# Kernel optimization log

Hardware: AMD Instinct MI355X
Metric: run time of the kernel (lower is better)

## Reference

```python
import math
import jax, jax.numpy as jnp
import numpy as np

B, L, D, I, S, DTR, K, PH = 8, 2048, 512, 256, 8, 32, 3, 128


def setup_inputs() -> dict:
    key = jax.random.key(0)
    ks = jax.random.split(key, 12)
    def nrm(k, shape, s=0.02):
        return jax.random.normal(k, shape, jnp.float32) * s
    # dt_proj bias: inverse-softplus of exp(linspace(log 0.02, log 0.2))
    dt_init = np.exp(np.linspace(math.log(0.02), math.log(0.2), I))
    dt_b = np.log(np.expm1(dt_init)).astype(np.float32)
    A_log = np.log(np.tile(np.arange(1, S + 1, dtype=np.float32), (I, 1)))
    return dict(
        x=jax.random.normal(ks[0], (B, L, D), jnp.float32),
        position=jax.random.uniform(ks[1], (B, L, 6), jnp.float32),
        ln_in_w=jnp.ones(D, jnp.float32), ln_in_b=jnp.zeros(D, jnp.float32),
        pos_w1=nrm(ks[2], (PH, 6), 0.1), pos_b1=jnp.zeros(PH, jnp.float32),
        pos_w2=nrm(ks[3], (D, PH), 0.05), pos_b2=jnp.zeros(D, jnp.float32),
        scan_in_w=nrm(ks[4], (2, D, D)),
        scan_cx_w=nrm(ks[5], (2, I, 1, K), 0.2),
        scan_cz_w=nrm(ks[6], (2, I, 1, K), 0.2),
        scan_xp_w=nrm(ks[7], (2, DTR + 2 * S, I)),
        scan_dt_w=nrm(ks[8], (2, I, DTR)),
        scan_dt_b=jnp.tile(jnp.asarray(dt_b)[None], (2, 1)),
        scan_Alog=jnp.tile(jnp.asarray(A_log)[None], (2, 1, 1)),
        scan_Dp=jnp.ones((2, I), jnp.float32),
        scan_out_w=nrm(ks[9], (2, D, D)),  # zero-init in source; randomized for non-trivial testing
        mix_w=nrm(ks[10], (D, 3 * D)),
        ln_out_w=jnp.ones(D, jnp.float32), ln_out_b=jnp.zeros(D, jnp.float32),
    )


def _ln(x, w, b, eps=1e-6):
    m = x.mean(-1, keepdims=True)
    v = ((x - m) ** 2).mean(-1, keepdims=True)
    return (x - m) * jax.lax.rsqrt(v + eps) * w + b


def _dwconv_silu(x, w):
    # x: [B, L, C], w: [C, 1, K] depthwise conv1d, 'same' padding, then SiLU
    y = jax.lax.conv_general_dilated(
        jnp.swapaxes(x, 1, 2), w, (1,), ((K // 2, K // 2),),
        feature_group_count=w.shape[0], dimension_numbers=('NCH', 'OIH', 'NCH'))
    return jax.nn.silu(jnp.swapaxes(y, 1, 2))


def _selective_scan(x, in_w, cx_w, cz_w, xp_w, dt_w, dt_b, Alog, Dp, out_w):
    # ReferenceSelectiveScan1D.forward, x: [B, L, D]
    xb, zb = jnp.split(x @ in_w.T, 2, axis=-1)
    xb = _dwconv_silu(xb, cx_w)
    zb = _dwconv_silu(zb, cz_w)
    proj = xb @ xp_w.T  # [B, L, DTR + 2S]
    dt_raw, b_raw, c_raw = jnp.split(proj, [DTR, DTR + S], axis=-1)
    delta = jnp.clip(jax.nn.softplus(dt_raw @ dt_w.T + dt_b), 1e-4, 1.0)  # [B, L, I]
    bt = jnp.tanh(b_raw)  # [B, L, S]
    ct = jnp.tanh(c_raw)  # [B, L, S]
    a = jax.nn.softplus(Alog) + 1e-4  # [I, S]
    xs = (jnp.swapaxes(delta, 0, 1), jnp.swapaxes(bt, 0, 1),
          jnp.swapaxes(ct, 0, 1), jnp.swapaxes(xb, 0, 1))

    def step(state, inp):
        d_t, b_t, c_t, x_t = inp
        decay = jnp.clip(jnp.exp(-d_t[..., None] * a), 1e-4, 1.0)  # [B, I, S]
        state = decay * state + (1.0 - decay) * (b_t[:, None, :] * x_t[..., None])
        y = jnp.einsum('bis,bs->bi', state, c_t) + Dp * x_t
        return state, y

    state0 = jnp.zeros((x.shape[0], I, S), jnp.float32)
    _, ys = jax.lax.scan(step, state0, xs)  # ys: [L, B, I]
    y = jnp.swapaxes(ys, 0, 1)
    return jnp.concatenate([y, zb], -1) @ out_w.T


def reference(x, position, ln_in_w, ln_in_b, pos_w1, pos_b1, pos_w2, pos_b2,
              scan_in_w, scan_cx_w, scan_cz_w, scan_xp_w, scan_dt_w, scan_dt_b,
              scan_Alog, scan_Dp, scan_out_w, mix_w, ln_out_w, ln_out_b):
    pos = jax.nn.gelu(position @ pos_w1.T + pos_b1, approximate=False) @ pos_w2.T + pos_b2
    si = _ln(x, ln_in_w, ln_in_b) + pos
    params = lambda i: (scan_in_w[i], scan_cx_w[i], scan_cz_w[i], scan_xp_w[i],
                        scan_dt_w[i], scan_dt_b[i], scan_Alog[i], scan_Dp[i], scan_out_w[i])
    fwd = _selective_scan(si, *params(0))
    bwd = jnp.flip(_selective_scan(jnp.flip(si, 1), *params(1)), 1)
    mixed = jnp.concatenate([fwd, bwd, si], -1) @ mix_w.T
    return _ln(mixed, ln_out_w, ln_out_b)
```

## Files before the change

### kernel.cpp

```cpp
#include <hip/hip_runtime.h>
#include <hip/hip_bf16.h>

typedef __hip_bfloat16 bf16;
typedef __attribute__((ext_vector_type(8))) short short8;
typedef __attribute__((ext_vector_type(4))) float floatx4;

#define BBB 8
#define LL 2048
#define DDD 512
#define II 256
#define SS 8
#define MM (BBB*LL)
#define CHUNK 32
#define NCH (LL/CHUNK)

#define WS_SI    0l
#define WS_U0    16777216l
#define WS_U1    33554432l
#define WS_XZ    50331648l
#define WS_H     67108864l
#define WS_P     50331648l
#define WS_Q     58720256l
#define WS_SINB  67108864l
#define WS_XBC   83886080l
#define WS_MIXED 83886080l
#define WS_DELTA 100663296l
#define WS_BTCT  117440512l
#define WS_INWB  121634816l
#define WS_MIXWB 122683392l
#define WS_PW2B  124256256l
#define WS_OWT   124387328l
#define WS_WP    125435904l
#define WS_WD    126484480l
#define WS_XPWB  126746624l
#define WS_A2    126763008l
#define WS_WXT   126779392l
#define WS_WZT   126785536l
#define WS_MRS   126791680l
#define WS_LNBP  126922752l

__device__ __forceinline__ float b2f(unsigned short u) {
    return __uint_as_float(((unsigned)u) << 16);
}
__device__ __forceinline__ float bload(const bf16* p) {
    return b2f(*(const unsigned short*)p);
}
__device__ __forceinline__ void bstore(bf16* p, float v) {
    *p = __float2bfloat16(v);
}
__device__ __forceinline__ float softplus_f(float x) {
    return fmaxf(x, 0.f) + log1pf(expf(-fabsf(x)));
}
__device__ __forceinline__ float silu_f(float x) {
    return x / (1.f + expf(-x));
}
__device__ __forceinline__ void gl_lds16(const bf16* g, void* l) {
    __builtin_amdgcn_global_load_lds(
        (const __attribute__((address_space(1))) unsigned int*)g,
        (__attribute__((address_space(3))) unsigned int*)l, 16, 0, 0);
}
#define VMWAIT8() asm volatile("s_waitcnt vmcnt(8)" ::: "memory")
#define VMWAIT0() asm volatile("s_waitcnt vmcnt(0)" ::: "memory")
#define XBAR()    __builtin_amdgcn_s_barrier()

__device__ __forceinline__ void block_mean_rstd(float v0, float v1, float* red,
                                                float& mean, float& rstd) {
    float s = v0 + v1, q = v0*v0 + v1*v1;
    #pragma unroll
    for (int off = 32; off > 0; off >>= 1) {
        s += __shfl_down(s, off);
        q += __shfl_down(q, off);
    }
    int w = threadIdx.x >> 6, lane = threadIdx.x & 63;
    if (lane == 0) { red[w*2] = s; red[w*2+1] = q; }
    __syncthreads();
    if (threadIdx.x == 0) {
        float ts = 0.f, tq = 0.f;
        #pragma unroll
        for (int i = 0; i < 4; ++i) { ts += red[i*2]; tq += red[i*2+1]; }
        red[8] = ts; red[9] = tq;
    }
    __syncthreads();
    float ts = red[8], tq = red[9];
    mean = ts * (1.f/DDD);
    float var = tq * (1.f/DDD) - mean*mean;
    rstd = rsqrtf(var + 1e-6f);
}

__global__ __launch_bounds__(256)
void k_prep(const float* __restrict__ x, float* __restrict__ mrs,
            const float* __restrict__ lnb, const float* __restrict__ pb2,
            float* __restrict__ lnbp,
            const float* __restrict__ position, const float* __restrict__ pw1,
            const float* __restrict__ pb1, bf16* __restrict__ H,
            const float* __restrict__ ow, bf16* __restrict__ owT,
            const float* __restrict__ mixw, bf16* __restrict__ mixwb,
            const float* __restrict__ inw, bf16* __restrict__ inwb,
            const float* __restrict__ dtw, const float* __restrict__ xpw,
            bf16* __restrict__ Wd,
            const float* __restrict__ posw2, bf16* __restrict__ pw2b,
            bf16* __restrict__ xpwb,
            const float* __restrict__ Alog, float* __restrict__ a2,
            const float* __restrict__ cxw, const float* __restrict__ czw,
            float* __restrict__ wxT, float* __restrict__ wzT) {
    __shared__ float red[10];
    int bb = blockIdx.x;
    int tid = threadIdx.x;
    if (bb < 16384) {
        long row = bb;
        float v0 = x[row*DDD + tid], v1 = x[row*DDD + tid + 256];
        float mean, rstd;
        block_mean_rstd(v0, v1, red, mean, rstd);
        if (tid == 0) { mrs[row*2] = mean; mrs[row*2+1] = rstd; }
    } else if (bb < 24576) {
        long idx = (long)(bb - 16384)*256 + tid;
        long row = idx >> 7; int ph = idx & 127;
        const float* p = position + row*6;
        const float* w = pw1 + ph*6;
        float v = pb1[ph];
        #pragma unroll
        for (int j = 0; j < 6; ++j) v = fmaf(p[j], w[j], v);
        v = 0.5f * v * (1.f + erff(v * 0.70710678118654752440f));
        bstore(H + idx, v);
    } else if (bb < 26624) {
        long idx = (long)(bb - 24576)*256 + tid;
        long d = idx >> 18; long rem = idx & 262143;
        long k = rem >> 9, c = rem & 511;
        bstore(owT + idx, ow[d*262144 + c*512 + k]);
    } else if (bb < 27392) {
        int i = (bb - 26624)*256*4 + tid*4;
        float4 v = *(const float4*)(mixw + i);
        bf16 t[4] = {__float2bfloat16(v.x), __float2bfloat16(v.y),
                     __float2bfloat16(v.z), __float2bfloat16(v.w)};
        *(ushort4*)(mixwb + i) = *(ushort4*)t;
    } else if (bb < 27904) {
        int i = (bb - 27392)*256*4 + tid*4;
        float4 v = *(const float4*)(inw + i);
        bf16 t[4] = {__float2bfloat16(v.x), __float2bfloat16(v.y),
                     __float2bfloat16(v.z), __float2bfloat16(v.w)};
        *(ushort4*)(inwb + i) = *(ushort4*)t;
    } else if (bb < 28416) {
        int local = bb - 27904;
        int d = local >> 8, i = local & 255, j = tid;
        const float* wr = dtw + (long)d*II*32 + i*32;
        const float* xp = xpw + (long)d*48*II;
        float acc = 0.f;
        #pragma unroll
        for (int k = 0; k < 32; ++k) acc = fmaf(wr[k], xp[k*II + j], acc);
        bstore(Wd + ((long)d*II + i)*II + j, acc);
    } else if (bb < 28480) {
        int i = (bb - 28416)*256*4 + tid*4;
        float4 v = *(const float4*)(posw2 + i);
        bf16 t[4] = {__float2bfloat16(v.x), __float2bfloat16(v.y),
                     __float2bfloat16(v.z), __float2bfloat16(v.w)};
        *(ushort4*)(pw2b + i) = *(ushort4*)t;
    } else if (bb < 28512) {
        int idx = (bb - 28480)*256 + tid;
        int d = idx >> 12, rem = idx & 4095;
        bstore(xpwb + idx, xpw[(long)d*48*II + 32*II + rem]);
    } else if (bb < 28528) {
        int idx = (bb - 28512)*256 + tid;
        float a = softplus_f(Alog[idx]) + 1e-4f;
        a2[idx] = -1.4426950408889634f * a;
    } else if (bb < 28534) {
        int idx = (bb - 28528)*256 + tid;
        if (idx < 1536) {
            int d = idx / 768, rem = idx % 768;
            int k = rem >> 8, i = rem & 255;
            int kk = d ? (2 - k) : k;
            wxT[idx] = cxw[d*768 + i*3 + kk];
            wzT[idx] = czw[d*768 + i*3 + kk];
        }
    } else {
        int idx = (bb - 28534)*256 + tid;
        lnbp[idx] = lnb[idx] + pb2[idx];
    }
}

#define GEMM_COMPUTE(Sa, Sb)                                                      \
    do {                                                                          \
        _Pragma("unroll")                                                         \
        for (int kk = 0; kk < 2; ++kk) {                                          \
            const int sa_ = ((kk*4 + lq) ^ (lr & 7)) * 16;                        \
            short8 af[4], bfr[4];                                                 \
            _Pragma("unroll")                                                     \
            for (int mi = 0; mi < 4; ++mi)                                        \
                af[mi] = *(const short8*)((const char*)&Sa[wm*64 + mi*16 + lr][0] + sa_); \
            _Pragma("unroll")                                                     \
            for (int ni = 0; ni < 4; ++ni)                                        \
                bfr[ni] = *(const short8*)((const char*)&Sb[wn*64 + ni*16 + lr][0] + sa_); \
            _Pragma("unroll")                                                     \
            for (int mi = 0; mi < 4; ++mi)                                        \
                _Pragma("unroll")                                                 \
                for (int ni = 0; ni < 4; ++ni)                                    \
                    acc[mi][ni] = __builtin_amdgcn_mfma_f32_16x16x32_bf16(        \
                        af[mi], bfr[ni], acc[mi][ni], 0, 0, 0);                   \
        }                                                                         \
    } while (0)

template<typename TC, int EPI = 0>
__global__ __launch_bounds__(256)
void gemm_mfma(const bf16* __restrict__ A, long lda,
               const bf16* __restrict__ B, long ldb,
               TC* __restrict__ C, long ldc, int Kdim,
               const float* __restrict__ bias,
               long zA, long zB, long zC, long zbias,
               const float* __restrict__ xf, const float* __restrict__ mrs,
               const float* __restrict__ lnw, const float* __restrict__ lnbp) {
    __shared__ short As0[128][64], Bs0[128][64];
    __shared__ short As1[128][64], Bs1[128][64];
    const int tid = threadIdx.x;
    const int lane = tid & 63;
    const int wave = tid >> 6;
    const int wm = wave >> 1, wn = wave & 1;
    const int lr = lane & 15, lq = lane >> 4;
    A += (long)blockIdx.z * zA;
    B += (long)blockIdx.z * zB;
    C += (long)blockIdx.z * zC;
    const float* bp = bias ? bias + (long)blockIdx.z * zbias : nullptr;
    int nwg = gridDim.x * gridDim.y;
    int bid = blockIdx.y * gridDim.x + blockIdx.x;
    int wg = (bid & 7) * (nwg >> 3) + (bid >> 3);
    const long m0 = (long)(wg / gridDim.x) * 128;
    const long n0 = (long)(wg % gridDim.x) * 128;

    const bf16* gA[4]; const bf16* gB[4]; int off16[4];
    #pragma unroll
    for (int q = 0; q < 4; ++q) {
        int ch = q*256 + tid;
        int r = ch >> 3;
        int g = (ch & 7) ^ (r & 7);
        gA[q] = A + (m0 + r)*lda + g*8;
        gB[q] = B + (n0 + r)*ldb + g*8;
        off16[q] = (q*256 + wave*64) * 16;
    }
#define STAGE_G(Sa, Sb, k0)                                   \
    do {                                                      \
        _Pragma("unroll")                                     \
        for (int q = 0; q < 4; ++q) {                         \
            gl_lds16(gA[q] + (k0), (char*)(Sa) + off16[q]);   \
            gl_lds16(gB[q] + (k0), (char*)(Sb) + off16[q]);   \
        }                                                     \
    } while (0)

    floatx4 acc[4][4];
    #pragma unroll
    for (int i = 0; i < 4; ++i)
        #pragma unroll
        for (int j = 0; j < 4; ++j)
            acc[i][j] = (floatx4){0.f, 0.f, 0.f, 0.f};

    const int NT = Kdim >> 6;
    STAGE_G(As0, Bs0, 0);
    STAGE_G(As1, Bs1, 64);
    int t = 0;
    for (; t + 2 < NT; t += 2) {
        VMWAIT8(); XBAR();
        GEMM_COMPUTE(As0, Bs0);
        XBAR();
        STAGE_G(As0, Bs0, (long)(t + 2) << 6);
        VMWAIT8(); XBAR();
        GEMM_COMPUTE(As1, Bs1);
        XBAR();
        STAGE_G(As1, Bs1, (long)(t + 3) << 6);
    }
    VMWAIT8(); XBAR();
    GEMM_COMPUTE(As0, Bs0);
    VMWAIT0(); XBAR();
    GEMM_COMPUTE(As1, Bs1);
#undef STAGE_G
    #pragma unroll
    for (int mi = 0; mi < 4; ++mi)
        #pragma unroll
        for (int ni = 0; ni < 4; ++ni)
            #pragma unroll
            for (int r = 0; r < 4; ++r) {
                long row = m0 + wm*64 + mi*16 + lq*4 + r;
                long col = n0 + wn*64 + ni*16 + lr;
                float v = acc[mi][ni][r];
                if (EPI == 1)
                    v = fminf(fmaxf(softplus_f(v + bp[col]), 1e-4f), 1.0f);
                if (EPI == 2) {
                    float2 ms = *(const float2*)(mrs + row*2);
                    v += (xf[row*512 + col] - ms.x)*ms.y*lnw[col] + lnbp[col];
                }
                if constexpr (sizeof(TC) == 2) bstore((bf16*)C + row*ldc + col, v);
                else ((float*)C)[row*ldc + col] = v;
            }
}

__global__ __launch_bounds__(256) void k_btct(const bf16* __restrict__ xbc,
                                              const bf16* __restrict__ xpwb,
                                              float* __restrict__ btct) {
    int d = blockIdx.y;
    int wave = threadIdx.x >> 6, lane = threadIdx.x & 63;
    long r0 = (long)blockIdx.x*64 + wave*16;
    int lr = lane & 15, lq = lane >> 4;
    const bf16* xb = xbc  + (long)d*MM*II;
    const bf16* wp = xpwb + (long)d*16*II;
    floatx4 acc = (floatx4){0.f, 0.f, 0.f, 0.f};
    #pragma unroll
    for (int k0 = 0; k0 < II; k0 += 32) {
        short8 af = *(const short8*)(xb + (r0 + lr)*II + k0 + lq*8);
        short8 bf = *(const short8*)(wp + lr*II + k0 + lq*8);
        acc = __builtin_amdgcn_mfma_f32_16x16x32_bf16(af, bf, acc, 0, 0, 0);
    }
    #pragma unroll
    for (int r = 0; r < 4; ++r) {
        long row = r0 + lq*4 + r;
        btct[((long)d*MM + row)*16 + lr] = tanhf(acc[r]);
    }
}

__global__ __launch_bounds__(256) void k_conv(const bf16* __restrict__ xz,
                                              const float* __restrict__ wxT,
                                              const float* __restrict__ wzT,
                                              bf16* __restrict__ xbc,
                                              bf16* __restrict__ u0,
                                              bf16* __restrict__ u1) {
    int d = blockIdx.y;
    long idx = (long)blockIdx.x*256 + threadIdx.x;
    long rg = idx >> 5; int i = (int)(idx & 31) * 8;
    long row0 = rg << 2;
    int l0 = (int)(row0 & (LL-1));
    const float* wxp = wxT + d*768 + i;
    const float* wzp = wzT + d*768 + i;
    float wxr[3][8], wzr[3][8];
    #pragma unroll
    for (int k = 0; k < 3; ++k) {
        *(float4*)&wxr[k][0] = *(const float4*)(wxp + k*256);
        *(float4*)&wxr[k][4] = *(const float4*)(wxp + k*256 + 4);
        *(float4*)&wzr[k][0] = *(const float4*)(wzp + k*256);
        *(float4*)&wzr[k][4] = *(const float4*)(wzp + k*256 + 4);
    }
    const bf16* base = xz + row0*1024 + (long)d*512 + i;
    short8 X[6], Z[6];
    #pragma unroll
    for (int k = 0; k < 6; ++k) {
        int gl = l0 - 1 + k;
        bool ok = (gl >= 0) && (gl < LL);
        if (ok) {
            X[k] = *(const short8*)(base + (long)(k-1)*1024);
            Z[k] = *(const short8*)(base + (long)(k-1)*1024 + 256);
        } else {
            X[k] = (short8){0,0,0,0,0,0,0,0};
            Z[k] = (short8){0,0,0,0,0,0,0,0};
        }
    }
    bf16* u = d ? u1 : u0;
    #pragma unroll
    for (int r = 0; r < 4; ++r) {
        bf16 ox[8], oz[8];
        #pragma unroll
        for (int j = 0; j < 8; ++j) {
            float ax = 0.f, az = 0.f;
            #pragma unroll
            for (int k = 0; k < 3; ++k) {
                ax = fmaf(b2f((unsigned short)X[r+k][j]), wxr[k][j], ax);
                az = fmaf(b2f((unsigned short)Z[r+k][j]), wzr[k][j], az);
            }
            ox[j] = __float2bfloat16(silu_f(ax));
            oz[j] = __float2bfloat16(silu_f(az));
        }
        *(short8*)(xbc + (long)d*MM*II + (row0+r)*II + i) = *(short8*)ox;
        *(short8*)(u + (row0+r)*512 + 256 + i) = *(short8*)oz;
    }
}

__global__ __launch_bounds__(256)
void gemm_mix3(const bf16* __restrict__ A0, const bf16* __restrict__ A1,
               const bf16* __restrict__ A2,
               const bf16* __restrict__ B0, const bf16* __restrict__ B1,
               const bf16* __restrict__ B2, long ldb2,
               bf16* __restrict__ C) {
    __shared__ short As0[128][64], Bs0[128][64];
    __shared__ short As1[128][64], Bs1[128][64];
    const int tid = threadIdx.x;
    const int lane = tid & 63;
    const int wave = tid >> 6;
    const int wm = wave >> 1, wn = wave & 1;
    const int lr = lane & 15, lq = lane >> 4;
    int nwg = gridDim.x * gridDim.y;
    int bid = blockIdx.y * gridDim.x + blockIdx.x;
    int wg = (bid & 7) * (nwg >> 3) + (bid >> 3);
    const long m0 = (long)(wg / gridDim.x) * 128;
    const long n0 = (long)(wg % gridDim.x) * 128;

    long aoff[4], boffA[4], boffB[4]; int off16[4];
    #pragma unroll
    for (int q = 0; q < 4; ++q) {
        int ch = q*256 + tid;
        int r = ch >> 3;
        int g = (ch & 7) ^ (r & 7);
        aoff[q]  = (m0 + r)*512 + g*8;
        boffA[q] = (n0 + r)*512 + g*8;
        boffB[q] = (n0 + r)*ldb2 + g*8;
        off16[q] = (q*256 + wave*64) * 16;
    }
#define STAGE_M(Sa, Sb, t)                                                   \
    do {                                                                     \
        int seg_ = (t) >> 3;                                                 \
        long kc_ = ((long)(t) << 6) & 511;                                   \
        const bf16* Ap_ = (seg_ == 0) ? A0 : (seg_ == 1 ? A1 : A2);          \
        const bf16* Bp_ = (seg_ == 0) ? B0 : (seg_ == 1 ? B1 : B2);          \
        _Pragma("unroll")                                                    \
        for (int q = 0; q < 4; ++q) {                                        \
            gl_lds16(Ap_ + aoff[q] + kc_, (char*)(Sa) + off16[q]);           \
            gl_lds16(Bp_ + (seg_ < 2 ? boffA[q] : boffB[q]) + kc_,           \
                     (char*)(Sb) + off16[q]);                                \
        }                                                                    \
    } while (0)

    floatx4 acc[4][4];
    #pragma unroll
    for (int i = 0; i < 4; ++i)
        #pragma unroll
        for (int j = 0; j < 4; ++j)
            acc[i][j] = (floatx4){0.f, 0.f, 0.f, 0.f};

    STAGE_M(As0, Bs0, 0);
    STAGE_M(As1, Bs1, 1);
    int t = 0;
    for (; t + 2 < 24; t += 2) {
        VMWAIT8(); XBAR();
        GEMM_COMPUTE(As0, Bs0);
        XBAR();
        STAGE_M(As0, Bs0, t + 2);
        VMWAIT8(); XBAR();
        GEMM_COMPUTE(As1, Bs1);
        XBAR();
        STAGE_M(As1, Bs1, t + 3);
    }
    VMWAIT8(); XBAR();
    GEMM_COMPUTE(As0, Bs0);
    VMWAIT0(); XBAR();
    GEMM_COMPUTE(As1, Bs1);
#undef STAGE_M
    #pragma unroll
    for (int mi = 0; mi < 4; ++mi)
        #pragma unroll
        for (int ni = 0; ni < 4; ++ni)
            #pragma unroll
            for (int r = 0; r < 4; ++r) {
                long row = m0 + wm*64 + mi*16 + lq*4 + r;
                long col = n0 + wn*64 + ni*16 + lr;
                bstore(C + row*512 + col, acc[mi][ni][r]);
            }
}

__global__ __launch_bounds__(256) void k_scan1(const bf16* __restrict__ delta,
                                               const float* __restrict__ btct,
                                               const bf16* __restrict__ xbc,
                                               const float* __restrict__ a2,
                                               float* __restrict__ P,
                                               float* __restrict__ Q) {
    __shared__ float bts[CHUNK][8];
    int z = blockIdx.y;
    int d = z >> 3, b = z & 7;
    int c = blockIdx.x;
    int i = threadIdx.x;
    {
        int tt = threadIdx.x >> 3, s = threadIdx.x & 7;
        int t = c*CHUNK + tt;
        long l = d ? (LL-1-t) : t;
        long row = (long)b*LL + l;
        bts[tt][s] = btct[(long)d*MM*16 + row*16 + s];
    }
    const float* ap = a2 + ((long)d*II + i)*8;
    float4 aA = *(const float4*)(ap);
    float4 aB = *(const float4*)(ap + 4);
    float a2r[8] = {aA.x, aA.y, aA.z, aA.w, aB.x, aB.y, aB.z, aB.w};
    __syncthreads();

    int t0 = c*CHUNK;
    long l0 = d ? (long)(LL-1-t0) : (long)t0;
    long row0 = (long)b*LL + l0;
    long step = (d ? -1l : 1l) * II;
    const bf16* pd = delta + (long)d*MM*II + row0*II + i;
    const bf16* px = xbc   + (long)d*MM*II + row0*II + i;

    float Pv[8], Qv[8];
    #pragma unroll
    for (int s = 0; s < 8; ++s) { Pv[s] = 1.f; Qv[s] = 0.f; }

    float dv = bload(pd), xv = bload(px);
    for (int tt = 0; tt < CHUNK; ++tt) {
        float dvn = 0.f, xvn = 0.f;
        if (tt + 1 < CHUNK) { dvn = bload(pd + step); xvn = bload(px + step); }
        pd += step; px += step;
        float4 b0 = *(const float4*)&bts[tt][0];
        float4 b1 = *(const float4*)&bts[tt][4];
        float btv[8] = {b0.x, b0.y, b0.z, b0.w, b1.x, b1.y, b1.z, b1.w};
        #pragma unroll
        for (int s = 0; s < 8; ++s) {
            float dec = __builtin_amdgcn_fmed3f(exp2f(dv*a2r[s]), 1e-4f, 1.0f);
            Pv[s] *= dec;
            Qv[s] = fmaf(dec, Qv[s], (1.f - dec)*btv[s]*xv);
        }
        dv = dvn; xv = xvn;
    }
    long o = ((long)z*NCH + c)*2048 + (long)i*8;
    *(floatx4*)(P + o)     = (floatx4){Pv[0], Pv[1], Pv[2], Pv[3]};
    *(floatx4*)(P + o + 4) = (floatx4){Pv[4], Pv[5], Pv[6], Pv[7]};
    *(floatx4*)(Q + o)     = (floatx4){Qv[0], Qv[1], Qv[2], Qv[3]};
    *(floatx4*)(Q + o + 4) = (floatx4){Qv[4], Qv[5], Qv[6], Qv[7]};
}

__global__ __launch_bounds__(256) void k_scan2(const float* __restrict__ P,
                                               const float* __restrict__ Q,
                                               float* __restrict__ sinb) {
    int d = blockIdx.y;
    long idx = (long)blockIdx.x*256 + threadIdx.x;
    int b = (int)(idx >> 11); int rem = (int)(idx & 2047);
    long base = ((long)(d*8 + b)*NCH)*2048 + rem;
    float st = 0.f;
    for (int c = 0; c < NCH; ++c) {
        long o = base + (long)c*2048;
        sinb[o] = st;
        st = fmaf(P[o], st, Q[o]);
    }
}

__global__ __launch_bounds__(256) void k_scan3(const bf16* __restrict__ delta,
                                               const float* __restrict__ btct,
                                               const bf16* __restrict__ xbc,
                                               const float* __restrict__ a2,
                                               const float* __restrict__ Dp,
                                               const float* __restrict__ sinb,
                                               bf16* __restrict__ u0,
                                               bf16* __restrict__ u1) {
    __shared__ float bcs[CHUNK][16];
    int z = blockIdx.y;
    int d = z >> 3, b = z & 7;
    int c = blockIdx.x;
    int i = threadIdx.x;
    {
        int tt = threadIdx.x >> 3, col = (threadIdx.x & 7)*2;
        int t = c*CHUNK + tt;
        long l = d ? (LL-1-t) : t;
        long row = (long)b*LL + l;
        *(float2*)&bcs[tt][col] =
            *(const float2*)(btct + (long)d*MM*16 + row*16 + col);
    }
    const float* ap = a2 + ((long)d*II + i)*8;
    float4 aA = *(const float4*)(ap);
    float4 aB = *(const float4*)(ap + 4);
    float a2r[8] = {aA.x, aA.y, aA.z, aA.w, aB.x, aB.y, aB.z, aB.w};
    float dpv = Dp[d*II + i];
    const float* sb = sinb + ((long)z*NCH + c)*2048 + (long)i*8;
    float4 s0 = *(const float4*)(sb);
    float4 s1 = *(const float4*)(sb + 4);
    float st[8] = {s0.x, s0.y, s0.z, s0.w, s1.x, s1.y, s1.z, s1.w};
    __syncthreads();

    int t0 = c*CHUNK;
    long l0 = d ? (long)(LL-1-t0) : (long)t0;
    long row0 = (long)b*LL + l0;
    long step = (d ? -1l : 1l) * II;
    long ustep = (d ? -1l : 1l) * 512;
    const bf16* pd = delta + (long)d*MM*II + row0*II + i;
    const bf16* px = xbc   + (long)d*MM*II + row0*II + i;
    bf16* pu = (d ? u1 : u0) + row0*512 + i;

    float dv = bload(pd), xv = bload(px);
    for (int tt = 0; tt < CHUNK; ++tt) {
        float dvn = 0.f, xvn = 0.f;
        if (tt + 1 < CHUNK) { dvn = bload(pd + step); xvn = bload(px + step); }
        pd += step; px += step;
        const float4* q4 = (const float4*)&bcs[tt][0];
        float4 b0 = q4[0], b1 = q4[1], c0 = q4[2], c1 = q4[3];
        float btv[8] = {b0.x, b0.y, b0.z, b0.w, b1.x, b1.y, b1.z, b1.w};
        float ctv[8] = {c0.x, c0.y, c0.z, c0.w, c1.x, c1.y, c1.z, c1.w};
        float pa = dpv * xv;
        #pragma unroll
        for (int s = 0; s < 8; ++s) {
            float dec = __builtin_amdgcn_fmed3f(exp2f(dv*a2r[s]), 1e-4f, 1.0f);
            st[s] = fmaf(dec, st[s], (1.f - dec)*btv[s]*xv);
            pa = fmaf(st[s], ctv[s], pa);
        }
        bstore(pu, pa);
        pu += ustep;
        dv = dvn; xv = xvn;
    }
}

__global__ __launch_bounds__(256) void k_ln_out(const bf16* __restrict__ mixed,
                                                const float* __restrict__ w,
                                                const float* __restrict__ b,
                                                float* __restrict__ out) {
    __shared__ float red[10];
    long row = blockIdx.x; int t = threadIdx.x;
    float v0 = bload(mixed + row*DDD + t), v1 = bload(mixed + row*DDD + t + 256);
    float mean, rstd;
    block_mean_rstd(v0, v1, red, mean, rstd);
    out[row*DDD + t]       = (v0-mean)*rstd*w[t]     + b[t];
    out[row*DDD + t + 256] = (v1-mean)*rstd*w[t+256] + b[t+256];
}

extern "C" void kernel_launch(void* const* d_in, const int* in_sizes, int n_in,
                              void* d_out, int out_size, void* d_ws, size_t ws_size,
                              hipStream_t stream) {
    const float* x        = (const float*)d_in[0];
    const float* position = (const float*)d_in[1];
    const float* ln_in_w  = (const float*)d_in[2];
    const float* ln_in_b  = (const float*)d_in[3];
    const float* pos_w1   = (const float*)d_in[4];
    const float* pos_b1   = (const float*)d_in[5];
    const float* pos_w2   = (const float*)d_in[6];
    const float* pos_b2   = (const float*)d_in[7];
    const float* in_w     = (const float*)d_in[8];
    const float* cx_w     = (const float*)d_in[9];
    const float* cz_w     = (const float*)d_in[10];
    const float* xp_w     = (const float*)d_in[11];
    const float* dt_w     = (const float*)d_in[12];
    const float* dt_b     = (const float*)d_in[13];
    const float* Alog     = (const float*)d_in[14];
    const float* Dp       = (const float*)d_in[15];
    const float* out_w    = (const float*)d_in[16];
    const float* mix_w    = (const float*)d_in[17];
    const float* ln_out_w = (const float*)d_in[18];
    const float* ln_out_b = (const float*)d_in[19];
    float* out = (float*)d_out;

    char* base = (char*)d_ws;
    bf16*  si     = (bf16*)(base + WS_SI);
    bf16*  u0     = (bf16*)(base + WS_U0);
    bf16*  u1     = (bf16*)(base + WS_U1);
    bf16*  xz     = (bf16*)(base + WS_XZ);
    bf16*  H      = (bf16*)(base + WS_H);
    float* Pb     = (float*)(base + WS_P);
    float* Qb     = (float*)(base + WS_Q);
    float* sinb   = (float*)(base + WS_SINB);
    bf16*  xbc    = (bf16*)(base + WS_XBC);
    bf16*  delta  = (bf16*)(base + WS_DELTA);
    float* btct   = (float*)(base + WS_BTCT);
    bf16*  mixed  = (bf16*)(base + WS_MIXED);
    bf16*  in_wb  = (bf16*)(base + WS_INWB);
    bf16*  mix_wb = (bf16*)(base + WS_MIXWB);
    bf16*  pw2b   = (bf16*)(base + WS_PW2B);
    bf16*  owT    = (bf16*)(base + WS_OWT);
    bf16*  Wp     = (bf16*)(base + WS_WP);
    bf16*  Wd     = (bf16*)(base + WS_WD);
    bf16*  xpwb   = (bf16*)(base + WS_XPWB);
    float* a2     = (float*)(base + WS_A2);
    float* wxT    = (float*)(base + WS_WXT);
    float* wzT    = (float*)(base + WS_WZT);
    float* mrs    = (float*)(base + WS_MRS);
    float* lnbp   = (float*)(base + WS_LNBP);

    k_prep<<<28536, 256, 0, stream>>>(x, mrs, ln_in_b, pos_b2, lnbp,
                                      position, pos_w1, pos_b1, H,
                                      out_w, owT, mix_w, mix_wb, in_w, in_wb,
                                      dt_w, xp_w, Wd, pos_w2, pw2b, xpwb,
                                      Alog, a2, cx_w, cz_w, wxT, wzT);
    gemm_mfma<bf16, 0><<<dim3(4, 4, 2), 256, 0, stream>>>(
        mix_wb, 1536, owT, 512, Wp, 512, 512, nullptr, 512, 262144, 262144, 0,
        nullptr, nullptr, nullptr, nullptr);
    gemm_mfma<bf16, 2><<<dim3(4, MM/128), 256, 0, stream>>>(
        H, 128, pw2b, 128, si, 512, 128, nullptr, 0, 0, 0, 0,
        x, mrs, ln_in_w, lnbp);
    gemm_mfma<bf16, 0><<<dim3(8, MM/128), 256, 0, stream>>>(
        si, 512, in_wb, 512, xz, 1024, 512, nullptr, 0, 0, 0, 0,
        nullptr, nullptr, nullptr, nullptr);
    k_conv<<<dim3(512, 2), 256, 0, stream>>>(xz, wxT, wzT, xbc, u0, u1);
    gemm_mfma<bf16, 1><<<dim3(2, MM/128, 2), 256, 0, stream>>>(
        xbc, 256, Wd, 256, delta, 256, 256, dt_b,
        (long)MM*II, 65536, (long)MM*II, 256,
        nullptr, nullptr, nullptr, nullptr);
    k_btct<<<dim3(MM/64, 2), 256, 0, stream>>>(xbc, xpwb, btct);
    k_scan1<<<dim3(NCH, 16), 256, 0, stream>>>(delta, btct, xbc, a2, Pb, Qb);
    k_scan2<<<dim3(64, 2), 256, 0, stream>>>(Pb, Qb, sinb);
    k_scan3<<<dim3(NCH, 16), 256, 0, stream>>>(delta, btct, xbc, a2, Dp,
                                               sinb, u0, u1);
    gemm_mix3<<<dim3(4, MM/128), 256, 0, stream>>>(u0, u1, si,
                                                   Wp, Wp + 262144, mix_wb + 1024, 1536,
                                                   mixed);
    k_ln_out<<<MM, 256, 0, stream>>>(mixed, ln_out_w, ln_out_b, out);
}
```

Baseline: 350.5 us.

## Double scan chunk size, cache bf16 copy of x, unroll carry pass

Raises the scan chunk length from 32 to 64, which halves the number of chunks the sequential carry pass in k_scan2 must walk and generalizes the per-chunk staging loops to match. k_prep now also writes a bf16 copy of x into the delta buffer region, so the positional GEMM epilogue reads bf16 instead of fp32 when reapplying the input layer norm. k_scan2 is unrolled by four with the loads hoisted ahead of the dependent fma chain. The wait macro is generalized and the GEMM inner loop gets constant parameters with no behavior change. Longer chunks lengthen the serial work per thread in scan1 and scan3 and may cut the number of blocks, and the bf16 copy of x slightly lowers the precision of the layer-norm term.

New measurement: 341.9 us. -2.4%, faster.

```diff
diff --git a/kernel.cpp b/kernel.cpp
--- a/kernel.cpp
+++ b/kernel.cpp
@@ -11,7 +11,7 @@
 #define II 256
 #define SS 8
 #define MM (BBB*LL)
-#define CHUNK 32
+#define CHUNK 64
 #define NCH (LL/CHUNK)
 
 #define WS_SI    0l
@@ -59,7 +59,7 @@
         (const __attribute__((address_space(1))) unsigned int*)g,
         (__attribute__((address_space(3))) unsigned int*)l, 16, 0, 0);
 }
-#define VMWAIT8() asm volatile("s_waitcnt vmcnt(8)" ::: "memory")
+#define VMWAIT_N(n) asm volatile("s_waitcnt vmcnt(" #n ")" ::: "memory")
 #define VMWAIT0() asm volatile("s_waitcnt vmcnt(0)" ::: "memory")
 #define XBAR()    __builtin_amdgcn_s_barrier()
 
@@ -89,6 +89,7 @@
 
 __global__ __launch_bounds__(256)
 void k_prep(const float* __restrict__ x, float* __restrict__ mrs,
+            bf16* __restrict__ xb16,
             const float* __restrict__ lnb, const float* __restrict__ pb2,
             float* __restrict__ lnbp,
             const float* __restrict__ position, const float* __restrict__ pw1,
@@ -109,6 +110,8 @@
     if (bb < 16384) {
         long row = bb;
         float v0 = x[row*DDD + tid], v1 = x[row*DDD + tid + 256];
+        bstore(xb16 + row*DDD + tid, v0);
+        bstore(xb16 + row*DDD + tid + 256, v1);
         float mean, rstd;
         block_mean_rstd(v0, v1, red, mean, rstd);
         if (tid == 0) { mrs[row*2] = mean; mrs[row*2+1] = rstd; }
@@ -180,8 +183,8 @@
 #define GEMM_COMPUTE(Sa, Sb)                                                      \
     do {                                                                          \
         _Pragma("unroll")                                                         \
-        for (int kk = 0; kk < 2; ++kk) {                                          \
-            const int sa_ = ((kk*4 + lq) ^ (lr & 7)) * 16;                        \
+        for (int kk = 0; kk < KKN; ++kk) {                                        \
+            const int sa_ = ((kk*4 + lq) ^ (lr & MASKC)) * 16;                    \
             short8 af[4], bfr[4];                                                 \
             _Pragma("unroll")                                                     \
             for (int mi = 0; mi < 4; ++mi)                                        \
@@ -205,8 +208,9 @@
                TC* __restrict__ C, long ldc, int Kdim,
                const float* __restrict__ bias,
                long zA, long zB, long zC, long zbias,
-               const float* __restrict__ xf, const float* __restrict__ mrs,
+               const bf16* __restrict__ xb16, const float* __restrict__ mrs,
                const float* __restrict__ lnw, const float* __restrict__ lnbp) {
+    enum { KKN = 2, MASKC = 7 };
     __shared__ short As0[128][64], Bs0[128][64];
     __shared__ short As1[128][64], Bs1[128][64];
     const int tid = threadIdx.x;
@@ -255,16 +259,16 @@
     STAGE_G(As1, Bs1, 64);
     int t = 0;
     for (; t + 2 < NT; t += 2) {
-        VMWAIT8(); XBAR();
+        VMWAIT_N(8); XBAR();
         GEMM_COMPUTE(As0, Bs0);
         XBAR();
         STAGE_G(As0, Bs0, (long)(t + 2) << 6);
-        VMWAIT8(); XBAR();
+        VMWAIT_N(8); XBAR();
         GEMM_COMPUTE(As1, Bs1);
         XBAR();
         STAGE_G(As1, Bs1, (long)(t + 3) << 6);
     }
-    VMWAIT8(); XBAR();
+    VMWAIT_N(8); XBAR();
     GEMM_COMPUTE(As0, Bs0);
     VMWAIT0(); XBAR();
     GEMM_COMPUTE(As1, Bs1);
@@ -282,7 +286,7 @@
                     v = fminf(fmaxf(softplus_f(v + bp[col]), 1e-4f), 1.0f);
                 if (EPI == 2) {
                     float2 ms = *(const float2*)(mrs + row*2);
-                    v += (xf[row*512 + col] - ms.x)*ms.y*lnw[col] + lnbp[col];
+                    v += (bload(xb16 + row*512 + col) - ms.x)*ms.y*lnw[col] + lnbp[col];
                 }
                 if constexpr (sizeof(TC) == 2) bstore((bf16*)C + row*ldc + col, v);
                 else ((float*)C)[row*ldc + col] = v;
@@ -373,6 +377,7 @@
                const bf16* __restrict__ B0, const bf16* __restrict__ B1,
                const bf16* __restrict__ B2, long ldb2,
                bf16* __restrict__ C) {
+    enum { KKN = 2, MASKC = 7 };
     __shared__ short As0[128][64], Bs0[128][64];
     __shared__ short As1[128][64], Bs1[128][64];
     const int tid = threadIdx.x;
@@ -422,16 +427,16 @@
     STAGE_M(As1, Bs1, 1);
     int t = 0;
     for (; t + 2 < 24; t += 2) {
-        VMWAIT8(); XBAR();
+        VMWAIT_N(8); XBAR();
         GEMM_COMPUTE(As0, Bs0);
         XBAR();
         STAGE_M(As0, Bs0, t + 2);
-        VMWAIT8(); XBAR();
+        VMWAIT_N(8); XBAR();
         GEMM_COMPUTE(As1, Bs1);
         XBAR();
         STAGE_M(As1, Bs1, t + 3);
     }
-    VMWAIT8(); XBAR();
+    VMWAIT_N(8); XBAR();
     GEMM_COMPUTE(As0, Bs0);
     VMWAIT0(); XBAR();
     GEMM_COMPUTE(As1, Bs1);
@@ -459,8 +464,10 @@
     int d = z >> 3, b = z & 7;
     int c = blockIdx.x;
     int i = threadIdx.x;
-    {
-        int tt = threadIdx.x >> 3, s = threadIdx.x & 7;
+    #pragma unroll
+    for (int q = 0; q < (CHUNK*8)/256; ++q) {
+        int t2 = q*256 + threadIdx.x;
+        int tt = t2 >> 3, s = t2 & 7;
         int t = c*CHUNK + tt;
         long l = d ? (LL-1-t) : t;
         long row = (long)b*LL + l;
@@ -514,10 +521,16 @@
     int b = (int)(idx >> 11); int rem = (int)(idx & 2047);
     long base = ((long)(d*8 + b)*NCH)*2048 + rem;
     float st = 0.f;
-    for (int c = 0; c < NCH; ++c) {
-        long o = base + (long)c*2048;
-        sinb[o] = st;
-        st = fmaf(P[o], st, Q[o]);
+    #pragma unroll 1
+    for (int c = 0; c < NCH; c += 4) {
+        long o0 = base + (long)c*2048;
+        long o1 = o0 + 2048, o2 = o0 + 4096, o3 = o0 + 6144;
+        float p0 = P[o0], p1 = P[o1], p2 = P[o2], p3 = P[o3];
+        float q0 = Q[o0], q1 = Q[o1], q2 = Q[o2], q3 = Q[o3];
+        sinb[o0] = st; st = fmaf(p0, st, q0);
+        sinb[o1] = st; st = fmaf(p1, st, q1);
+        sinb[o2] = st; st = fmaf(p2, st, q2);
+        sinb[o3] = st; st = fmaf(p3, st, q3);
     }
 }
 
@@ -534,8 +547,10 @@
     int d = z >> 3, b = z & 7;
     int c = blockIdx.x;
     int i = threadIdx.x;
-    {
-        int tt = threadIdx.x >> 3, col = (threadIdx.x & 7)*2;
+    #pragma unroll
+    for (int q = 0; q < (CHUNK*16)/512; ++q) {
+        int t2 = q*256 + threadIdx.x;
+        int tt = t2 >> 3, col = (t2 & 7)*2;
         int t = c*CHUNK + tt;
         long l = d ? (LL-1-t) : t;
         long row = (long)b*LL + l;
@@ -633,6 +648,7 @@
     float* sinb   = (float*)(base + WS_SINB);
     bf16*  xbc    = (bf16*)(base + WS_XBC);
     bf16*  delta  = (bf16*)(base + WS_DELTA);
+    bf16*  xb16   = (bf16*)(base + WS_DELTA);
     float* btct   = (float*)(base + WS_BTCT);
     bf16*  mixed  = (bf16*)(base + WS_MIXED);
     bf16*  in_wb  = (bf16*)(base + WS_INWB);
@@ -648,7 +664,7 @@
     float* mrs    = (float*)(base + WS_MRS);
     float* lnbp   = (float*)(base + WS_LNBP);
 
-    k_prep<<<28536, 256, 0, stream>>>(x, mrs, ln_in_b, pos_b2, lnbp,
+    k_prep<<<28536, 256, 0, stream>>>(x, mrs, xb16, ln_in_b, pos_b2, lnbp,
                                       position, pos_w1, pos_b1, H,
                                       out_w, owT, mix_w, mix_wb, in_w, in_wb,
                                       dt_w, xp_w, Wd, pos_w2, pw2b, xpwb,
@@ -658,7 +674,7 @@
         nullptr, nullptr, nullptr, nullptr);
     gemm_mfma<bf16, 2><<<dim3(4, MM/128), 256, 0, stream>>>(
         H, 128, pw2b, 128, si, 512, 128, nullptr, 0, 0, 0, 0,
-        x, mrs, ln_in_w, lnbp);
+        xb16, mrs, ln_in_w, lnbp);
     gemm_mfma<bf16, 0><<<dim3(8, MM/128), 256, 0, stream>>>(
         si, 512, in_wb, 512, xz, 1024, 512, nullptr, 0, 0, 0, 0,
         nullptr, nullptr, nullptr, nullptr);
```
